# Kernel optimization log

Measured on AMD Instinct MI355X. Metric: run time of the kernel, lower is better.

## Reference

```python
import jax, jax.numpy as jnp
import numpy as np

PLANES = 128
SCALE = float(np.sqrt(PLANES))
TEMP = 0.05


def _maxpool2x2(x):
    # x: [B, C, H, W] -> [B, C, H//2, W//2]
    return jax.lax.reduce_window(x, -jnp.inf, jax.lax.max,
                                 (1, 1, 2, 2), (1, 1, 2, 2), 'VALID')


def _conv1x1(x, w, b=None):
    # x: [B, Cin, H, W], w: [Cout, Cin]
    y = jnp.einsum('bchw,oc->bohw', x, w)
    if b is not None:
        y = y + b[None, :, None, None]
    return y


def setup_inputs() -> dict:
    key = jax.random.key(0)
    ks = jax.random.split(key, 9)
    B, C, H, W = 8, 512, 64, 64
    std = 0.01  # init.normal_(w, 0, 0.01)
    x = jax.random.normal(ks[0], (B, C, H, W), dtype=jnp.float32)
    wq = jax.random.normal(ks[1], (PLANES, C), dtype=jnp.float32) * std
    bq = jnp.zeros((PLANES,), dtype=jnp.float32)
    wk = jax.random.normal(ks[2], (PLANES, C), dtype=jnp.float32) * std
    bk = jnp.zeros((PLANES,), dtype=jnp.float32)
    wv = jax.random.normal(ks[3], (C, C), dtype=jnp.float32) * std  # no bias (use_out=False)
    wm = jax.random.normal(ks[4], (1, C), dtype=jnp.float32) * std
    bm = jnp.zeros((1,), dtype=jnp.float32)
    # torch inits gamma to zero; use a nonzero value so the attention path matters
    gamma = jax.random.normal(ks[5], (1,), dtype=jnp.float32)
    return {'x': x, 'wq': wq, 'bq': bq, 'wk': wk, 'bk': bk,
            'wv': wv, 'wm': wm, 'bm': bm, 'gamma': gamma}


def reference(x, wq, bq, wk, bk, wv, wm, bm, gamma):
    B, C, H, W = x.shape
    xd = _maxpool2x2(x)                                   # [B,C,H/2,W/2]
    Hm, Wm = xd.shape[2], xd.shape[3]
    N, M = H * W, Hm * Wm
    q = _conv1x1(x, wq, bq).reshape(B, PLANES, N)         # [B,P,N]
    k = _conv1x1(xd, wk, bk).reshape(B, PLANES, M)        # [B,P,M]
    v = _conv1x1(xd, wv).reshape(B, C, M)                 # [B,C,M]
    # 'channel' whitening: subtract per-channel spatial mean
    q = q - q.mean(axis=2, keepdims=True)
    k = k - k.mean(axis=2, keepdims=True)
    sim = jnp.einsum('bpn,bpm->bnm', q, k) / (SCALE * TEMP)  # [B,N,M]
    sim = jax.nn.softmax(sim, axis=2)
    out_sim = jnp.einsum('bnm,bcm->bcn', sim, v).reshape(B, C, H, W)
    out_sim = gamma[0] * out_sim
    # global-context branch (with_gc, no 2fc)
    mask = _conv1x1(xd, wm, bm).reshape(B, M)             # [B,M]
    mask = jax.nn.softmax(mask, axis=1)
    out_gc = jnp.einsum('bcm,bm->bc', v, mask)[:, :, None, None]  # [B,C,1,1]
    return out_sim + out_gc + x
```

## Files before the change

kernel.cpp:

```cpp
#include <hip/hip_runtime.h>

typedef float f32x4 __attribute__((ext_vector_type(4)));
typedef short bf16x8 __attribute__((ext_vector_type(8)));
typedef short s16x4 __attribute__((ext_vector_type(4)));
typedef unsigned short u16;

#define B_ 8
#define C_ 512
#define N_ 4096
#define M_ 1024
#define P_ 128
#define INV_ST 1.7677669529663689f
#define A2C 2.5506631384888954f
#define B2C 23.083120654223414f

#define MFMA __builtin_amdgcn_mfma_f32_16x16x32_bf16

__device__ __forceinline__ u16 f2b(float f) {
  unsigned u = __float_as_uint(f);
  u += 0x7fffu + ((u >> 16) & 1u);
  return (u16)(u >> 16);
}
__device__ __forceinline__ float b2f(u16 h) {
  return __uint_as_float(((unsigned)h) << 16);
}
__device__ __forceinline__ float waveRedSum(float v) {
#pragma unroll
  for (int off = 32; off > 0; off >>= 1) v += __shfl_xor(v, off);
  return v;
}
__device__ __forceinline__ void gload_lds16(const u16* g, u16* l) {
  __builtin_amdgcn_global_load_lds(
      (const __attribute__((address_space(1))) void*)g,
      (__attribute__((address_space(3))) void*)l, 16, 0, 0);
}

__global__ __launch_bounds__(256) void prep_pool(const float* __restrict__ x,
                                                 float* __restrict__ xd,
                                                 float* __restrict__ meanx,
                                                 float* __restrict__ meanxd) {
  const int bc = blockIdx.x;
  const int tid = threadIdx.x;
  const int lane = tid & 63, wid = tid >> 6;
  const float* xp = x + (size_t)bc * 4096;
  float* xdp = xd + (size_t)bc * 1024;
  __shared__ float xs[4096];
  __shared__ float w4[4], w4b[4];
  float s = 0.f;
#pragma unroll
  for (int i = 0; i < 16; ++i) {
    float v = xp[i * 256 + tid];
    xs[i * 256 + tid] = v;
    s += v;
  }
  s = waveRedSum(s);
  if (lane == 0) w4[wid] = s;
  __syncthreads();
  if (tid == 0) meanx[bc] = (w4[0] + w4[1] + w4[2] + w4[3]) * (1.f / 4096.f);
  float sd = 0.f;
#pragma unroll
  for (int i = 0; i < 4; ++i) {
    int mp = i * 256 + tid;
    int r2 = mp >> 5, c2 = mp & 31;
    const float* p0 = xs + r2 * 128 + c2 * 2;
    float v = fmaxf(fmaxf(p0[0], p0[1]), fmaxf(p0[64], p0[65]));
    xdp[mp] = v;
    sd += v;
  }
  sd = waveRedSum(sd);
  if (lane == 0) w4b[wid] = sd;
  __syncthreads();
  if (tid == 0) meanxd[bc] = (w4b[0] + w4b[1] + w4b[2] + w4b[3]) * (1.f / 1024.f);
}

__global__ __launch_bounds__(256) void f2bf3(const float* __restrict__ a,
                                             const float* __restrict__ b,
                                             const float* __restrict__ c,
                                             u16* __restrict__ oa,
                                             u16* __restrict__ ob,
                                             u16* __restrict__ oc) {
  int i = blockIdx.x * 256 + threadIdx.x;
  if (i < 65536) oa[i] = f2b(a[i]);
  else if (i < 131072) ob[i - 65536] = f2b(b[i - 65536]);
  else if (i < 393216) oc[i - 131072] = f2b(c[i - 131072]);
}

template <int ROWS, bool TRANS, bool SUBMEAN>
__global__ __launch_bounds__(256) void gemm_wx(const u16* __restrict__ A,
                                               const float* __restrict__ Bsrc,
                                               const float* __restrict__ mean,
                                               u16* __restrict__ outp,
                                               int Cout, int Ncols) {
  constexpr int IT = ROWS / 32;
  const int b = blockIdx.z;
  const int col0 = blockIdx.x * 64;
  const int row0 = blockIdx.y * ROWS;
  const int tid = threadIdx.x;
  const int lane = tid & 63, wid = tid >> 6;
  const int g = lane >> 4, c16 = lane & 15;
  const int wr = (wid >> 1) * (ROWS / 2), wc = (wid & 1) * 32;
  __shared__ __align__(16) u16 As[ROWS][72];
  __shared__ __align__(16) u16 Bt[64][72];
  const float* Bb = Bsrc + (size_t)b * 512 * Ncols;
  const float* mb = SUBMEAN ? (mean + b * 512) : nullptr;
  f32x4 acc[IT][2];
#pragma unroll
  for (int i = 0; i < IT; ++i)
#pragma unroll
    for (int j = 0; j < 2; ++j) acc[i][j] = (f32x4){0.f, 0.f, 0.f, 0.f};

  for (int k0 = 0; k0 < 512; k0 += 64) {
#pragma unroll
    for (int i = 0; i < IT; ++i) {
      int f = tid + i * 256;
      int r = f >> 3, c8 = f & 7;
      *(bf16x8*)&As[r][c8 * 8] =
          *(const bf16x8*)(A + (size_t)(row0 + r) * 512 + k0 + c8 * 8);
    }
#pragma unroll
    for (int i = 0; i < 4; ++i) {
      int f = tid + i * 256;
      int kr = f >> 4, n4 = (f & 15) * 4;
      const float* src = Bb + (size_t)(k0 + kr) * Ncols + col0 + n4;
      float4 val = *(const float4*)src;
      if (SUBMEAN) {
        float mv = mb[k0 + kr];
        val.x -= mv; val.y -= mv; val.z -= mv; val.w -= mv;
      }
      Bt[n4 + 0][kr] = f2b(val.x);
      Bt[n4 + 1][kr] = f2b(val.y);
      Bt[n4 + 2][kr] = f2b(val.z);
      Bt[n4 + 3][kr] = f2b(val.w);
    }
    __syncthreads();
#pragma unroll
    for (int kk = 0; kk < 2; ++kk) {
      bf16x8 bfr[2];
#pragma unroll
      for (int j = 0; j < 2; ++j)
        bfr[j] = *(const bf16x8*)&Bt[wc + j * 16 + c16][kk * 32 + g * 8];
#pragma unroll
      for (int i = 0; i < IT; ++i) {
        bf16x8 af = *(const bf16x8*)&As[wr + i * 16 + c16][kk * 32 + g * 8];
#pragma unroll
        for (int j = 0; j < 2; ++j)
          acc[i][j] = MFMA(af, bfr[j], acc[i][j], 0, 0, 0);
      }
    }
    __syncthreads();
  }
  if (TRANS) {
#pragma unroll
    for (int i = 0; i < IT; ++i)
#pragma unroll
      for (int j = 0; j < 2; ++j) {
        int row = row0 + wr + i * 16 + g * 4;
        int col = col0 + wc + j * 16 + c16;
        s16x4 h;
#pragma unroll
        for (int r = 0; r < 4; ++r) h[r] = (short)f2b(acc[i][j][r]);
        *(s16x4*)(outp + ((size_t)b * Ncols + col) * Cout + row) = h;
      }
  } else {
#pragma unroll
    for (int i = 0; i < IT; ++i)
#pragma unroll
      for (int j = 0; j < 2; ++j) {
        int row = row0 + wr + i * 16 + g * 4;
        int col = col0 + wc + j * 16 + c16;
#pragma unroll
        for (int r = 0; r < 4; ++r)
          outp[((size_t)b * Cout + row + r) * Ncols + col] = f2b(acc[i][j][r]);
      }
  }
}

__global__ __launch_bounds__(128) void k_logits(const float* __restrict__ xd,
                                                const float* __restrict__ wm,
                                                const float* __restrict__ bmp,
                                                float* __restrict__ logits) {
  const int b = blockIdx.x >> 5, mc = blockIdx.x & 31;
  const int t = threadIdx.x;
  const int ml = t & 31, cq = t >> 5;
  const int m = mc * 32 + ml;
  __shared__ float part[4][32];
  const float* xb = xd + (size_t)b * 512 * 1024 + m;
  float s0 = 0, s1 = 0, s2 = 0, s3 = 0;
  const int cb = cq * 128;
#pragma unroll 8
  for (int c = 0; c < 128; c += 4) {
    s0 += wm[cb + c + 0] * xb[(size_t)(cb + c + 0) * 1024];
    s1 += wm[cb + c + 1] * xb[(size_t)(cb + c + 1) * 1024];
    s2 += wm[cb + c + 2] * xb[(size_t)(cb + c + 2) * 1024];
    s3 += wm[cb + c + 3] * xb[(size_t)(cb + c + 3) * 1024];
  }
  part[cq][ml] = (s0 + s1) + (s2 + s3);
  __syncthreads();
  if (t < 32)
    logits[b * 1024 + mc * 32 + t] =
        part[0][t] + part[1][t] + part[2][t] + part[3][t] + bmp[0];
}

__global__ __launch_bounds__(256) void k_gc(const float* __restrict__ logits,
                                            const u16* __restrict__ v,
                                            float* __restrict__ gc) {
  const int b = blockIdx.x >> 4, cc = blockIdx.x & 15;
  const int tid = threadIdx.x;
  const int lane = tid & 63, wid = tid >> 6;
  __shared__ float pl[1024];
  __shared__ float r4[4];
  __shared__ float stot[2];
  float4 lv = *(const float4*)&logits[b * 1024 + tid * 4];
  float mx = fmaxf(fmaxf(lv.x, lv.y), fmaxf(lv.z, lv.w));
#pragma unroll
  for (int off = 32; off > 0; off >>= 1) mx = fmaxf(mx, __shfl_xor(mx, off));
  if (lane == 0) r4[wid] = mx;
  __syncthreads();
  if (tid == 0) stot[0] = fmaxf(fmaxf(r4[0], r4[1]), fmaxf(r4[2], r4[3]));
  __syncthreads();
  const float M = stot[0];
  float e0 = __expf(lv.x - M), e1 = __expf(lv.y - M);
  float e2 = __expf(lv.z - M), e3 = __expf(lv.w - M);
  pl[tid * 4 + 0] = e0; pl[tid * 4 + 1] = e1;
  pl[tid * 4 + 2] = e2; pl[tid * 4 + 3] = e3;
  float ps = waveRedSum((e0 + e1) + (e2 + e3));
  if (lane == 0) r4[wid] = ps;
  __syncthreads();
  if (tid == 0) stot[1] = 1.0f / (r4[0] + r4[1] + r4[2] + r4[3]);
  __syncthreads();
  const float inv = stot[1];
  const int c = cc * 32 + (tid >> 3), sub = tid & 7;
  const u16* vr = v + ((size_t)b * 512 + c) * 1024 + sub * 128;
  const float* plr = pl + sub * 128;
  float s = 0;
#pragma unroll
  for (int i = 0; i < 16; ++i) {
    bf16x8 h = *(const bf16x8*)(vr + i * 8);
#pragma unroll
    for (int j = 0; j < 8; ++j) s += b2f((u16)h[j]) * plr[i * 8 + j];
  }
  s += __shfl_xor(s, 1);
  s += __shfl_xor(s, 2);
  s += __shfl_xor(s, 4);
  if (sub == 0) gc[b * 512 + c] = s * inv;
}

__global__ __launch_bounds__(512, 2) void attn(const u16* __restrict__ q,
                                               const u16* __restrict__ kt,
                                               const u16* __restrict__ v,
                                               const float* __restrict__ gc,
                                               const float* __restrict__ x,
                                               const float* __restrict__ gamma,
                                               float* __restrict__ out) {
  extern __shared__ __align__(16) char smem[];
  u16* Vl = (u16*)smem;
  u16* Pl = (u16*)(smem + 131072);
  float* l_s = (float*)(smem + 139264);

  const int bid = blockIdx.x;
  const int b = bid & 7;
  const int n0 = (bid >> 3) * 64;
  const int tid = threadIdx.x;
  const int lane = tid & 63, wid = tid >> 6;
  const int g = lane >> 4, c16 = lane & 15;
  const int mb = wid & 3, nh = wid >> 2;
  const int xsw = (c16 & 7) << 3;

  bf16x8 qf[2][4];
  {
    const u16* qr = q + ((size_t)b * N_ + n0 + nh * 32 + c16) * P_ + g * 8;
#pragma unroll
    for (int t = 0; t < 2; ++t)
#pragma unroll
      for (int kf = 0; kf < 4; ++kf)
        qf[t][kf] = *(const bf16x8*)(qr + t * 16 * P_ + kf * 32);
  }
  const u16* ktr = kt + ((size_t)b * M_ + mb * 16 + c16) * P_ + g * 8;
  bf16x8 kb[2][4];
#pragma unroll
  for (int kf = 0; kf < 4; ++kf) kb[0][kf] = *(const bf16x8*)(ktr + kf * 32);
  const u16* vst = v + ((size_t)b * C_ + wid * 64 + (lane >> 3)) * M_ +
                   ((lane & 7) ^ (lane >> 3)) * 8;
#pragma unroll
  for (int i = 0; i < 8; ++i)
    gload_lds16(vst + (size_t)i * 8 * M_, Vl + (wid * 8 + i) * 512);

  f32x4 acc[4][4];
#pragma unroll
  for (int i = 0; i < 4; ++i)
#pragma unroll
    for (int j = 0; j < 4; ++j) acc[i][j] = (f32x4){0.f, 0.f, 0.f, 0.f};
  float lp0 = 0.f, lp1 = 0.f;

#pragma unroll
  for (int s = 0; s < 16; ++s) {
    const int par = s & 1, nxt = par ^ 1;
    const int m0n = ((s + 1) & 15) * 64;
    f32x4 sv0 = (f32x4){0.f, 0.f, 0.f, 0.f};
    f32x4 sv1 = (f32x4){0.f, 0.f, 0.f, 0.f};
#pragma unroll
    for (int kf = 0; kf < 4; ++kf) {
      sv0 = MFMA(kb[par][kf], qf[0][kf], sv0, 0, 0, 0);
      sv1 = MFMA(kb[par][kf], qf[1][kf], sv1, 0, 0, 0);
    }
    float p00 = exp2f(fmaf(sv0[0], A2C, -B2C));
    float p01 = exp2f(fmaf(sv0[1], A2C, -B2C));
    float p02 = exp2f(fmaf(sv0[2], A2C, -B2C));
    float p03 = exp2f(fmaf(sv0[3], A2C, -B2C));
    float p10 = exp2f(fmaf(sv1[0], A2C, -B2C));
    float p11 = exp2f(fmaf(sv1[1], A2C, -B2C));
    float p12 = exp2f(fmaf(sv1[2], A2C, -B2C));
    float p13 = exp2f(fmaf(sv1[3], A2C, -B2C));
    lp0 += (p00 + p01) + (p02 + p03);
    lp1 += (p10 + p11) + (p12 + p13);
    uint2 w0, w1;
    w0.x = (unsigned)f2b(p00) | ((unsigned)f2b(p01) << 16);
    w0.y = (unsigned)f2b(p02) | ((unsigned)f2b(p03) << 16);
    w1.x = (unsigned)f2b(p10) | ((unsigned)f2b(p11) << 16);
    w1.y = (unsigned)f2b(p12) | ((unsigned)f2b(p13) << 16);

    __builtin_amdgcn_sched_barrier(0);
    __builtin_amdgcn_s_barrier();
    __builtin_amdgcn_sched_barrier(0);
#pragma unroll
    for (int kf = 0; kf < 4; ++kf)
      kb[nxt][kf] = *(const bf16x8*)(ktr + (size_t)m0n * P_ + kf * 32);
#pragma unroll
    for (int i = 0; i < 8; ++i)
      gload_lds16(vst + (size_t)(m0n + i * 8 * M_),
                  Vl + nxt * 32768 + (wid * 8 + i) * 512);
    {
      const int nA = nh * 32 + c16;
      const int o = (mb * 16 + g * 4) ^ xsw;
      *(uint2*)&Pl[nA * 64 + o] = w0;
      *(uint2*)&Pl[(nA + 16) * 64 + o] = w1;
    }
    asm volatile("s_waitcnt vmcnt(12) lgkmcnt(0)" ::: "memory");
    __builtin_amdgcn_sched_barrier(0);
    __builtin_amdgcn_s_barrier();
    __builtin_amdgcn_sched_barrier(0);
    const u16* VlP = Vl + par * 32768;
#pragma unroll
    for (int kk = 0; kk < 2; ++kk) {
      bf16x8 pb[4];
#pragma unroll
      for (int nb = 0; nb < 4; ++nb)
        pb[nb] = *(const bf16x8*)&Pl[(nb * 16 + c16) * 64 + ((kk * 32 + g * 8) ^ xsw)];
#pragma unroll
      for (int cf = 0; cf < 4; ++cf) {
        bf16x8 va = *(const bf16x8*)&VlP[(wid * 64 + cf * 16 + c16) * 64 +
                                         ((kk * 32 + g * 8) ^ xsw)];
#pragma unroll
        for (int nb = 0; nb < 4; ++nb)
          acc[cf][nb] = MFMA(va, pb[nb], acc[cf][nb], 0, 0, 0);
      }
    }
  }

  lp0 += __shfl_xor(lp0, 16); lp0 += __shfl_xor(lp0, 32);
  lp1 += __shfl_xor(lp1, 16); lp1 += __shfl_xor(lp1, 32);
  if (lane < 16) {
    l_s[mb * 64 + nh * 32 + lane] = lp0;
    l_s[mb * 64 + nh * 32 + 16 + lane] = lp1;
  }
  __syncthreads();
  float linv[4];
#pragma unroll
  for (int nb = 0; nb < 4; ++nb) {
    int n = nb * 16 + c16;
    linv[nb] = 1.0f / (l_s[n] + l_s[64 + n] + l_s[128 + n] + l_s[192 + n]);
  }
  const float gam = gamma[0];
#pragma unroll
  for (int cf = 0; cf < 4; ++cf) {
    const int c = wid * 64 + cf * 16 + g * 4;
    float gcv[4];
#pragma unroll
    for (int r = 0; r < 4; ++r) gcv[r] = gc[b * C_ + c + r];
#pragma unroll
    for (int nb = 0; nb < 4; ++nb) {
      const size_t idx0 = ((size_t)b * C_ + c) * (size_t)N_ + n0 + nb * 16 + c16;
#pragma unroll
      for (int r = 0; r < 4; ++r) {
        const size_t idx = idx0 + (size_t)r * N_;
        out[idx] = gam * acc[cf][nb][r] * linv[nb] + gcv[r] + x[idx];
      }
    }
  }
}

extern "C" void kernel_launch(void* const* d_in, const int* in_sizes, int n_in,
                              void* d_out, int out_size, void* d_ws, size_t ws_size,
                              hipStream_t stream) {
  const float* x     = (const float*)d_in[0];
  const float* wq    = (const float*)d_in[1];
  const float* wk    = (const float*)d_in[3];
  const float* wv    = (const float*)d_in[5];
  const float* wm    = (const float*)d_in[6];
  const float* bm    = (const float*)d_in[7];
  const float* gamma = (const float*)d_in[8];
  float* out = (float*)d_out;
  char* ws = (char*)d_ws;

  float* xd     = (float*)(ws + 0);
  float* meanx  = (float*)(ws + 16777216);
  float* meanxd = (float*)(ws + 16793600);
  u16*   q_ws   = (u16*)(ws + 16809984);
  u16*   kt_ws  = (u16*)(ws + 25198592);
  u16*   v_ws   = (u16*)(ws + 27295744);
  u16*   wq_b   = (u16*)(ws + 35684352);
  u16*   wk_b   = (u16*)(ws + 35815424);
  u16*   wv_b   = (u16*)(ws + 35946496);
  float* gc     = (float*)(ws + 36470784);
  float* logits = (float*)(ws + 36487168);

  prep_pool<<<dim3(B_ * C_), dim3(256), 0, stream>>>(x, xd, meanx, meanxd);
  f2bf3<<<dim3(1536), dim3(256), 0, stream>>>(wq, wk, wv, wq_b, wk_b, wv_b);
  gemm_wx<128, true, true><<<dim3(64, 1, B_), dim3(256), 0, stream>>>(
      wq_b, x, meanx, q_ws, 128, 4096);
  gemm_wx<128, true, true><<<dim3(16, 1, B_), dim3(256), 0, stream>>>(
      wk_b, xd, meanxd, kt_ws, 128, 1024);
  gemm_wx<128, false, false><<<dim3(16, 4, B_), dim3(256), 0, stream>>>(
      wv_b, xd, nullptr, v_ws, 512, 1024);
  k_logits<<<dim3(256), dim3(128), 0, stream>>>(xd, wm, bm, logits);
  k_gc<<<dim3(128), dim3(256), 0, stream>>>(logits, v_ws, gc);

  hipFuncSetAttribute((const void*)attn,
                      hipFuncAttributeMaxDynamicSharedMemorySize, 140288);
  attn<<<dim3(512), dim3(512), 140288, stream>>>(q_ws, kt_ws, v_ws, gc, x,
                                                 gamma, out);
}
```

Baseline: 307.2 us.

## Pre-transpose x to bf16, fold mean subtraction into GEMM epilogue, software-pipeline attention

A new prep kernel transposes x and the pooled xd into channel-last bf16 buffers and accumulates the channel means with atomics. The q/k mean subtraction is now applied as a precomputed W·mean correction in the GEMM epilogue, so the GEMMs load bf16 operands directly with larger tiles. The mask-logit computation is merged into the weight-conversion kernel. The attention loop double-buffers P in LDS and computes the next tile's scores after the PV MMA, dropping one barrier per iteration. In exchange this adds an extra pass writing the transposed copies, atomics, a memset and more LDS in attention.

```diff
diff --git a/kernel.cpp b/kernel.cpp
--- a/kernel.cpp
+++ b/kernel.cpp
@@ -10,7 +10,6 @@
 #define N_ 4096
 #define M_ 1024
 #define P_ 128
-#define INV_ST 1.7677669529663689f
 #define A2C 2.5506631384888954f
 #define B2C 23.083120654223414f
 
@@ -35,115 +34,162 @@
       (__attribute__((address_space(3))) void*)l, 16, 0, 0);
 }
 
-__global__ __launch_bounds__(256) void prep_pool(const float* __restrict__ x,
-                                                 float* __restrict__ xd,
-                                                 float* __restrict__ meanx,
-                                                 float* __restrict__ meanxd) {
-  const int bc = blockIdx.x;
-  const int tid = threadIdx.x;
-  const int lane = tid & 63, wid = tid >> 6;
-  const float* xp = x + (size_t)bc * 4096;
-  float* xdp = xd + (size_t)bc * 1024;
-  __shared__ float xs[4096];
-  __shared__ float w4[4], w4b[4];
-  float s = 0.f;
-#pragma unroll
-  for (int i = 0; i < 16; ++i) {
-    float v = xp[i * 256 + tid];
-    xs[i * 256 + tid] = v;
-    s += v;
-  }
-  s = waveRedSum(s);
-  if (lane == 0) w4[wid] = s;
-  __syncthreads();
-  if (tid == 0) meanx[bc] = (w4[0] + w4[1] + w4[2] + w4[3]) * (1.f / 4096.f);
-  float sd = 0.f;
-#pragma unroll
-  for (int i = 0; i < 4; ++i) {
-    int mp = i * 256 + tid;
-    int r2 = mp >> 5, c2 = mp & 31;
-    const float* p0 = xs + r2 * 128 + c2 * 2;
-    float v = fmaxf(fmaxf(p0[0], p0[1]), fmaxf(p0[64], p0[65]));
-    xdp[mp] = v;
-    sd += v;
-  }
-  sd = waveRedSum(sd);
-  if (lane == 0) w4b[wid] = sd;
-  __syncthreads();
-  if (tid == 0) meanxd[bc] = (w4b[0] + w4b[1] + w4b[2] + w4b[3]) * (1.f / 1024.f);
-}
-
-__global__ __launch_bounds__(256) void f2bf3(const float* __restrict__ a,
-                                             const float* __restrict__ b,
-                                             const float* __restrict__ c,
-                                             u16* __restrict__ oa,
-                                             u16* __restrict__ ob,
-                                             u16* __restrict__ oc) {
-  int i = blockIdx.x * 256 + threadIdx.x;
-  if (i < 65536) oa[i] = f2b(a[i]);
-  else if (i < 131072) ob[i - 65536] = f2b(b[i - 65536]);
-  else if (i < 393216) oc[i - 131072] = f2b(c[i - 131072]);
-}
-
-template <int ROWS, bool TRANS, bool SUBMEAN>
-__global__ __launch_bounds__(256) void gemm_wx(const u16* __restrict__ A,
-                                               const float* __restrict__ Bsrc,
-                                               const float* __restrict__ mean,
+__global__ __launch_bounds__(256) void prep_tx(const float* __restrict__ x,
+                                               u16* __restrict__ xt,
+                                               u16* __restrict__ xdt,
+                                               float* __restrict__ meanx,
+                                               float* __restrict__ meanxd) {
+  const int bid = blockIdx.x;
+  const int b = bid >> 8, ct = (bid >> 5) & 7, hp = bid & 31;
+  const int t = threadIdx.x;
+  const int lane = t & 63, wid = t >> 6;
+  __shared__ float xs[64 * 133];
+  __shared__ float part[4][64];
+  const float* xb = x + ((size_t)(b * 512 + ct * 64) * 4096) + hp * 128;
+#pragma unroll
+  for (int it = 0; it < 32; ++it) {
+    int c = it * 2 + (t >> 7);
+    int n = t & 127;
+    xs[c * 133 + n] = xb[(size_t)c * 4096 + n];
+  }
+  __syncthreads();
+  {
+    int c = t >> 2, qq = t & 3;
+    float s = 0;
+#pragma unroll
+    for (int j = 0; j < 32; ++j) s += xs[c * 133 + qq * 32 + j];
+    s += __shfl_xor(s, 1);
+    s += __shfl_xor(s, 2);
+    if (qq == 0) atomicAdd(&meanx[b * 512 + ct * 64 + c], s * (1.f / 4096.f));
+  }
+#pragma unroll
+  for (int it = 0; it < 16; ++it) {
+    int n = it * 8 + (t >> 5), cp = t & 31;
+    float lo = xs[(2 * cp) * 133 + n], hi = xs[(2 * cp + 1) * 133 + n];
+    unsigned u = (unsigned)f2b(lo) | ((unsigned)f2b(hi) << 16);
+    *(unsigned*)(xt + (((size_t)b * 4096) + hp * 128 + n) * 512 + ct * 64 + 2 * cp) = u;
+  }
+  float s0 = 0, s1 = 0;
+  const int cp = t & 31;
+#pragma unroll
+  for (int it = 0; it < 4; ++it) {
+    int wm = it * 8 + (t >> 5);
+    int c0 = 2 * cp;
+    float a = fmaxf(fmaxf(xs[c0 * 133 + 2 * wm], xs[c0 * 133 + 2 * wm + 1]),
+                    fmaxf(xs[c0 * 133 + 64 + 2 * wm], xs[c0 * 133 + 64 + 2 * wm + 1]));
+    float d = fmaxf(fmaxf(xs[(c0 + 1) * 133 + 2 * wm], xs[(c0 + 1) * 133 + 2 * wm + 1]),
+                    fmaxf(xs[(c0 + 1) * 133 + 64 + 2 * wm], xs[(c0 + 1) * 133 + 64 + 2 * wm + 1]));
+    unsigned u = (unsigned)f2b(a) | ((unsigned)f2b(d) << 16);
+    *(unsigned*)(xdt + (((size_t)b * 1024) + hp * 32 + wm) * 512 + ct * 64 + c0) = u;
+    s0 += a; s1 += d;
+  }
+  s0 += __shfl_xor(s0, 32);
+  s1 += __shfl_xor(s1, 32);
+  if (lane < 32) { part[wid][2 * cp] = s0; part[wid][2 * cp + 1] = s1; }
+  __syncthreads();
+  if (t < 64)
+    atomicAdd(&meanxd[b * 512 + ct * 64 + t],
+              (part[0][t] + part[1][t] + part[2][t] + part[3][t]) * (1.f / 1024.f));
+}
+
+__global__ __launch_bounds__(256) void wcvt(const float* __restrict__ wq,
+                                            const float* __restrict__ wk,
+                                            const float* __restrict__ wv,
+                                            const float* __restrict__ wm,
+                                            const float* __restrict__ bm,
+                                            const float* __restrict__ meanx,
+                                            const float* __restrict__ meanxd,
+                                            const u16* __restrict__ xdt,
+                                            u16* __restrict__ wq_b,
+                                            u16* __restrict__ wk_b,
+                                            u16* __restrict__ wv_b,
+                                            float* __restrict__ corr_q,
+                                            float* __restrict__ corr_k,
+                                            float* __restrict__ logits) {
+  const int bid = blockIdx.x, t = threadIdx.x;
+  if (bid < 1536) {
+    int i = bid * 256 + t;
+    if (i < 65536) wq_b[i] = f2b(wq[i]);
+    else if (i < 131072) wk_b[i - 65536] = f2b(wk[i - 65536]);
+    else wv_b[i - 131072] = f2b(wv[i - 131072]);
+  } else if (bid < 1552) {
+    int blk = bid - 1536, b = blk & 7, sel = blk >> 3;
+    const float* w = sel ? wk : wq;
+    const float* mn = (sel ? meanxd : meanx) + b * 512;
+    int p = t >> 1, h = t & 1;
+    const float* wr = w + p * 512 + h * 256;
+    const float* mr = mn + h * 256;
+    float s = 0;
+#pragma unroll 8
+    for (int c = 0; c < 256; ++c) s += wr[c] * mr[c];
+    s += __shfl_xor(s, 1);
+    if (h == 0) (sel ? corr_k : corr_q)[b * 128 + p] = s;
+  } else {
+    int blk = bid - 1552;
+    int b = blk >> 8, mblk = blk & 255;
+    int lane = t & 63, wv4 = t >> 6;
+    int m = mblk * 4 + wv4;
+    bf16x8 h8 = *(const bf16x8*)(xdt + ((size_t)b * 1024 + m) * 512 + lane * 8);
+    const float* wmr = wm + lane * 8;
+    float s = 0;
+#pragma unroll
+    for (int j = 0; j < 8; ++j) s += b2f((u16)h8[j]) * wmr[j];
+    s = waveRedSum(s);
+    if (lane == 0) logits[b * 1024 + m] = s + bm[0];
+  }
+}
+
+template <int BR, int BC, bool TRANS, bool CORR>
+__global__ __launch_bounds__(256) void gemm_bt(const u16* __restrict__ A,
+                                               const u16* __restrict__ Bt,
+                                               const float* __restrict__ corr,
                                                u16* __restrict__ outp,
                                                int Cout, int Ncols) {
-  constexpr int IT = ROWS / 32;
+  constexpr int WR = BR / 2, WC = BC / 2, ITR = WR / 16, ITC = WC / 16;
+  constexpr int AFR = BR * 8 / 256, BFR = BC * 8 / 256;
   const int b = blockIdx.z;
-  const int col0 = blockIdx.x * 64;
-  const int row0 = blockIdx.y * ROWS;
+  const int col0 = blockIdx.x * BC;
+  const int row0 = blockIdx.y * BR;
   const int tid = threadIdx.x;
   const int lane = tid & 63, wid = tid >> 6;
   const int g = lane >> 4, c16 = lane & 15;
-  const int wr = (wid >> 1) * (ROWS / 2), wc = (wid & 1) * 32;
-  __shared__ __align__(16) u16 As[ROWS][72];
-  __shared__ __align__(16) u16 Bt[64][72];
-  const float* Bb = Bsrc + (size_t)b * 512 * Ncols;
-  const float* mb = SUBMEAN ? (mean + b * 512) : nullptr;
-  f32x4 acc[IT][2];
-#pragma unroll
-  for (int i = 0; i < IT; ++i)
-#pragma unroll
-    for (int j = 0; j < 2; ++j) acc[i][j] = (f32x4){0.f, 0.f, 0.f, 0.f};
+  const int wr = (wid >> 1) * WR, wc = (wid & 1) * WC;
+  __shared__ __align__(16) u16 As[BR][72];
+  __shared__ __align__(16) u16 Bs[BC][72];
+  const u16* Bb = Bt + (size_t)b * Ncols * 512;
+  f32x4 acc[ITR][ITC];
+#pragma unroll
+  for (int i = 0; i < ITR; ++i)
+#pragma unroll
+    for (int j = 0; j < ITC; ++j) acc[i][j] = (f32x4){0.f, 0.f, 0.f, 0.f};
 
   for (int k0 = 0; k0 < 512; k0 += 64) {
 #pragma unroll
-    for (int i = 0; i < IT; ++i) {
+    for (int i = 0; i < AFR; ++i) {
       int f = tid + i * 256;
       int r = f >> 3, c8 = f & 7;
       *(bf16x8*)&As[r][c8 * 8] =
           *(const bf16x8*)(A + (size_t)(row0 + r) * 512 + k0 + c8 * 8);
     }
 #pragma unroll
-    for (int i = 0; i < 4; ++i) {
+    for (int i = 0; i < BFR; ++i) {
       int f = tid + i * 256;
-      int kr = f >> 4, n4 = (f & 15) * 4;
-      const float* src = Bb + (size_t)(k0 + kr) * Ncols + col0 + n4;
-      float4 val = *(const float4*)src;
-      if (SUBMEAN) {
-        float mv = mb[k0 + kr];
-        val.x -= mv; val.y -= mv; val.z -= mv; val.w -= mv;
-      }
-      Bt[n4 + 0][kr] = f2b(val.x);
-      Bt[n4 + 1][kr] = f2b(val.y);
-      Bt[n4 + 2][kr] = f2b(val.z);
-      Bt[n4 + 3][kr] = f2b(val.w);
+      int r = f >> 3, c8 = f & 7;
+      *(bf16x8*)&Bs[r][c8 * 8] =
+          *(const bf16x8*)(Bb + (size_t)(col0 + r) * 512 + k0 + c8 * 8);
     }
     __syncthreads();
 #pragma unroll
     for (int kk = 0; kk < 2; ++kk) {
-      bf16x8 bfr[2];
-#pragma unroll
-      for (int j = 0; j < 2; ++j)
-        bfr[j] = *(const bf16x8*)&Bt[wc + j * 16 + c16][kk * 32 + g * 8];
-#pragma unroll
-      for (int i = 0; i < IT; ++i) {
+      bf16x8 bfr[ITC];
+#pragma unroll
+      for (int j = 0; j < ITC; ++j)
+        bfr[j] = *(const bf16x8*)&Bs[wc + j * 16 + c16][kk * 32 + g * 8];
+#pragma unroll
+      for (int i = 0; i < ITR; ++i) {
         bf16x8 af = *(const bf16x8*)&As[wr + i * 16 + c16][kk * 32 + g * 8];
 #pragma unroll
-        for (int j = 0; j < 2; ++j)
+        for (int j = 0; j < ITC; ++j)
           acc[i][j] = MFMA(af, bfr[j], acc[i][j], 0, 0, 0);
       }
     }
@@ -151,21 +197,25 @@
   }
   if (TRANS) {
 #pragma unroll
-    for (int i = 0; i < IT; ++i)
-#pragma unroll
-      for (int j = 0; j < 2; ++j) {
+    for (int i = 0; i < ITR; ++i)
+#pragma unroll
+      for (int j = 0; j < ITC; ++j) {
         int row = row0 + wr + i * 16 + g * 4;
         int col = col0 + wc + j * 16 + c16;
         s16x4 h;
 #pragma unroll
-        for (int r = 0; r < 4; ++r) h[r] = (short)f2b(acc[i][j][r]);
+        for (int r = 0; r < 4; ++r) {
+          float val = acc[i][j][r];
+          if (CORR) val -= corr[b * 128 + row + r];
+          h[r] = (short)f2b(val);
+        }
         *(s16x4*)(outp + ((size_t)b * Ncols + col) * Cout + row) = h;
       }
   } else {
 #pragma unroll
-    for (int i = 0; i < IT; ++i)
-#pragma unroll
-      for (int j = 0; j < 2; ++j) {
+    for (int i = 0; i < ITR; ++i)
+#pragma unroll
+      for (int j = 0; j < ITC; ++j) {
         int row = row0 + wr + i * 16 + g * 4;
         int col = col0 + wc + j * 16 + c16;
 #pragma unroll
@@ -173,32 +223,6 @@
           outp[((size_t)b * Cout + row + r) * Ncols + col] = f2b(acc[i][j][r]);
       }
   }
-}
-
-__global__ __launch_bounds__(128) void k_logits(const float* __restrict__ xd,
-                                                const float* __restrict__ wm,
-                                                const float* __restrict__ bmp,
-                                                float* __restrict__ logits) {
-  const int b = blockIdx.x >> 5, mc = blockIdx.x & 31;
-  const int t = threadIdx.x;
-  const int ml = t & 31, cq = t >> 5;
-  const int m = mc * 32 + ml;
-  __shared__ float part[4][32];
-  const float* xb = xd + (size_t)b * 512 * 1024 + m;
-  float s0 = 0, s1 = 0, s2 = 0, s3 = 0;
-  const int cb = cq * 128;
-#pragma unroll 8
-  for (int c = 0; c < 128; c += 4) {
-    s0 += wm[cb + c + 0] * xb[(size_t)(cb + c + 0) * 1024];
-    s1 += wm[cb + c + 1] * xb[(size_t)(cb + c + 1) * 1024];
-    s2 += wm[cb + c + 2] * xb[(size_t)(cb + c + 2) * 1024];
-    s3 += wm[cb + c + 3] * xb[(size_t)(cb + c + 3) * 1024];
-  }
-  part[cq][ml] = (s0 + s1) + (s2 + s3);
-  __syncthreads();
-  if (t < 32)
-    logits[b * 1024 + mc * 32 + t] =
-        part[0][t] + part[1][t] + part[2][t] + part[3][t] + bmp[0];
 }
 
 __global__ __launch_bounds__(256) void k_gc(const float* __restrict__ logits,
@@ -245,6 +269,35 @@
   if (sub == 0) gc[b * 512 + c] = s * inv;
 }
 
+__device__ __forceinline__ void s_phase(const bf16x8* kbf, const bf16x8 (&qf)[2][4],
+                                        u16* PlBuf, int nA, int o,
+                                        float& lp0, float& lp1) {
+  f32x4 sv0 = (f32x4){0.f, 0.f, 0.f, 0.f};
+  f32x4 sv1 = (f32x4){0.f, 0.f, 0.f, 0.f};
+#pragma unroll
+  for (int kf = 0; kf < 4; ++kf) {
+    sv0 = MFMA(kbf[kf], qf[0][kf], sv0, 0, 0, 0);
+    sv1 = MFMA(kbf[kf], qf[1][kf], sv1, 0, 0, 0);
+  }
+  float p00 = exp2f(fmaf(sv0[0], A2C, -B2C));
+  float p01 = exp2f(fmaf(sv0[1], A2C, -B2C));
+  float p02 = exp2f(fmaf(sv0[2], A2C, -B2C));
+  float p03 = exp2f(fmaf(sv0[3], A2C, -B2C));
+  float p10 = exp2f(fmaf(sv1[0], A2C, -B2C));
+  float p11 = exp2f(fmaf(sv1[1], A2C, -B2C));
+  float p12 = exp2f(fmaf(sv1[2], A2C, -B2C));
+  float p13 = exp2f(fmaf(sv1[3], A2C, -B2C));
+  lp0 += (p00 + p01) + (p02 + p03);
+  lp1 += (p10 + p11) + (p12 + p13);
+  uint2 w0, w1;
+  w0.x = (unsigned)f2b(p00) | ((unsigned)f2b(p01) << 16);
+  w0.y = (unsigned)f2b(p02) | ((unsigned)f2b(p03) << 16);
+  w1.x = (unsigned)f2b(p10) | ((unsigned)f2b(p11) << 16);
+  w1.y = (unsigned)f2b(p12) | ((unsigned)f2b(p13) << 16);
+  *(uint2*)&PlBuf[nA * 64 + o] = w0;
+  *(uint2*)&PlBuf[(nA + 16) * 64 + o] = w1;
+}
+
 __global__ __launch_bounds__(512, 2) void attn(const u16* __restrict__ q,
                                                const u16* __restrict__ kt,
                                                const u16* __restrict__ v,
@@ -255,8 +308,7 @@
   extern __shared__ __align__(16) char smem[];
   u16* Vl = (u16*)smem;
   u16* Pl = (u16*)(smem + 131072);
-  float* l_s = (float*)(smem + 139264);
-
+  float* l_s = (float*)(smem + 147456);
   const int bid = blockIdx.x;
   const int b = bid & 7;
   const int n0 = (bid >> 3) * 64;
@@ -265,6 +317,8 @@
   const int g = lane >> 4, c16 = lane & 15;
   const int mb = wid & 3, nh = wid >> 2;
   const int xsw = (c16 & 7) << 3;
+  const int nA = nh * 32 + c16;
+  const int po = (mb * 16 + g * 4) ^ xsw;
 
   bf16x8 qf[2][4];
   {
@@ -279,73 +333,53 @@
   bf16x8 kb[2][4];
 #pragma unroll
   for (int kf = 0; kf < 4; ++kf) kb[0][kf] = *(const bf16x8*)(ktr + kf * 32);
+#pragma unroll
+  for (int kf = 0; kf < 4; ++kf) kb[1][kf] = *(const bf16x8*)(ktr + 64 * P_ + kf * 32);
   const u16* vst = v + ((size_t)b * C_ + wid * 64 + (lane >> 3)) * M_ +
                    ((lane & 7) ^ (lane >> 3)) * 8;
 #pragma unroll
   for (int i = 0; i < 8; ++i)
     gload_lds16(vst + (size_t)i * 8 * M_, Vl + (wid * 8 + i) * 512);
 
+  float lp0 = 0.f, lp1 = 0.f;
+  s_phase(kb[0], qf, Pl, nA, po, lp0, lp1);
+
   f32x4 acc[4][4];
 #pragma unroll
   for (int i = 0; i < 4; ++i)
 #pragma unroll
     for (int j = 0; j < 4; ++j) acc[i][j] = (f32x4){0.f, 0.f, 0.f, 0.f};
-  float lp0 = 0.f, lp1 = 0.f;
-
-#pragma unroll
+
+#pragma unroll 2
   for (int s = 0; s < 16; ++s) {
     const int par = s & 1, nxt = par ^ 1;
-    const int m0n = ((s + 1) & 15) * 64;
-    f32x4 sv0 = (f32x4){0.f, 0.f, 0.f, 0.f};
-    f32x4 sv1 = (f32x4){0.f, 0.f, 0.f, 0.f};
-#pragma unroll
-    for (int kf = 0; kf < 4; ++kf) {
-      sv0 = MFMA(kb[par][kf], qf[0][kf], sv0, 0, 0, 0);
-      sv1 = MFMA(kb[par][kf], qf[1][kf], sv1, 0, 0, 0);
-    }
-    float p00 = exp2f(fmaf(sv0[0], A2C, -B2C));
-    float p01 = exp2f(fmaf(sv0[1], A2C, -B2C));
-    float p02 = exp2f(fmaf(sv0[2], A2C, -B2C));
-    float p03 = exp2f(fmaf(sv0[3], A2C, -B2C));
-    float p10 = exp2f(fmaf(sv1[0], A2C, -B2C));
-    float p11 = exp2f(fmaf(sv1[1], A2C, -B2C));
-    float p12 = exp2f(fmaf(sv1[2], A2C, -B2C));
-    float p13 = exp2f(fmaf(sv1[3], A2C, -B2C));
-    lp0 += (p00 + p01) + (p02 + p03);
-    lp1 += (p10 + p11) + (p12 + p13);
-    uint2 w0, w1;
-    w0.x = (unsigned)f2b(p00) | ((unsigned)f2b(p01) << 16);
-    w0.y = (unsigned)f2b(p02) | ((unsigned)f2b(p03) << 16);
-    w1.x = (unsigned)f2b(p10) | ((unsigned)f2b(p11) << 16);
-    w1.y = (unsigned)f2b(p12) | ((unsigned)f2b(p13) << 16);
-
+    if (s < 14) {
+      const size_t moff = (size_t)(s + 2) * 64 * P_;
+#pragma unroll
+      for (int kf = 0; kf < 4; ++kf)
+        kb[par][kf] = *(const bf16x8*)(ktr + moff + kf * 32);
+      asm volatile("s_waitcnt vmcnt(4) lgkmcnt(0)" ::: "memory");
+    } else {
+      asm volatile("s_waitcnt vmcnt(0) lgkmcnt(0)" ::: "memory");
+    }
     __builtin_amdgcn_sched_barrier(0);
     __builtin_amdgcn_s_barrier();
     __builtin_amdgcn_sched_barrier(0);
-#pragma unroll
-    for (int kf = 0; kf < 4; ++kf)
-      kb[nxt][kf] = *(const bf16x8*)(ktr + (size_t)m0n * P_ + kf * 32);
-#pragma unroll
-    for (int i = 0; i < 8; ++i)
-      gload_lds16(vst + (size_t)(m0n + i * 8 * M_),
-                  Vl + nxt * 32768 + (wid * 8 + i) * 512);
-    {
-      const int nA = nh * 32 + c16;
-      const int o = (mb * 16 + g * 4) ^ xsw;
-      *(uint2*)&Pl[nA * 64 + o] = w0;
-      *(uint2*)&Pl[(nA + 16) * 64 + o] = w1;
-    }
-    asm volatile("s_waitcnt vmcnt(12) lgkmcnt(0)" ::: "memory");
-    __builtin_amdgcn_sched_barrier(0);
-    __builtin_amdgcn_s_barrier();
-    __builtin_amdgcn_sched_barrier(0);
+    if (s < 15) {
+      const int m1 = (s + 1) * 64;
+#pragma unroll
+      for (int i = 0; i < 8; ++i)
+        gload_lds16(vst + m1 + (size_t)i * 8 * M_,
+                    Vl + nxt * 32768 + (wid * 8 + i) * 512);
+    }
     const u16* VlP = Vl + par * 32768;
+    const u16* PlP = Pl + par * 4096;
 #pragma unroll
     for (int kk = 0; kk < 2; ++kk) {
       bf16x8 pb[4];
 #pragma unroll
       for (int nb = 0; nb < 4; ++nb)
-        pb[nb] = *(const bf16x8*)&Pl[(nb * 16 + c16) * 64 + ((kk * 32 + g * 8) ^ xsw)];
+        pb[nb] = *(const bf16x8*)&PlP[(nb * 16 + c16) * 64 + ((kk * 32 + g * 8) ^ xsw)];
 #pragma unroll
       for (int cf = 0; cf < 4; ++cf) {
         bf16x8 va = *(const bf16x8*)&VlP[(wid * 64 + cf * 16 + c16) * 64 +
@@ -355,6 +389,7 @@
           acc[cf][nb] = MFMA(va, pb[nb], acc[cf][nb], 0, 0, 0);
       }
     }
+    if (s < 15) s_phase(kb[nxt], qf, Pl + nxt * 4096, nA, po, lp0, lp1);
   }
 
   lp0 += __shfl_xor(lp0, 16); lp0 += __shfl_xor(lp0, 32);
@@ -402,31 +437,36 @@
   float* out = (float*)d_out;
   char* ws = (char*)d_ws;
 
-  float* xd     = (float*)(ws + 0);
-  float* meanx  = (float*)(ws + 16777216);
-  float* meanxd = (float*)(ws + 16793600);
-  u16*   q_ws   = (u16*)(ws + 16809984);
-  u16*   kt_ws  = (u16*)(ws + 25198592);
-  u16*   v_ws   = (u16*)(ws + 27295744);
-  u16*   wq_b   = (u16*)(ws + 35684352);
-  u16*   wk_b   = (u16*)(ws + 35815424);
-  u16*   wv_b   = (u16*)(ws + 35946496);
-  float* gc     = (float*)(ws + 36470784);
-  float* logits = (float*)(ws + 36487168);
-
-  prep_pool<<<dim3(B_ * C_), dim3(256), 0, stream>>>(x, xd, meanx, meanxd);
-  f2bf3<<<dim3(1536), dim3(256), 0, stream>>>(wq, wk, wv, wq_b, wk_b, wv_b);
-  gemm_wx<128, true, true><<<dim3(64, 1, B_), dim3(256), 0, stream>>>(
-      wq_b, x, meanx, q_ws, 128, 4096);
-  gemm_wx<128, true, true><<<dim3(16, 1, B_), dim3(256), 0, stream>>>(
-      wk_b, xd, meanxd, kt_ws, 128, 1024);
-  gemm_wx<128, false, false><<<dim3(16, 4, B_), dim3(256), 0, stream>>>(
-      wv_b, xd, nullptr, v_ws, 512, 1024);
-  k_logits<<<dim3(256), dim3(128), 0, stream>>>(xd, wm, bm, logits);
+  u16*   xt     = (u16*)(ws + 0);
+  u16*   xdt    = (u16*)(ws + 33554432);
+  u16*   q_ws   = (u16*)(ws + 41943040);
+  u16*   kt_ws  = (u16*)(ws + 50331648);
+  u16*   v_ws   = (u16*)(ws + 52428800);
+  u16*   wq_b   = (u16*)(ws + 60817408);
+  u16*   wk_b   = (u16*)(ws + 60948480);
+  u16*   wv_b   = (u16*)(ws + 61079552);
+  float* meanx  = (float*)(ws + 61603840);
+  float* meanxd = (float*)(ws + 61620224);
+  float* corr_q = (float*)(ws + 61636608);
+  float* corr_k = (float*)(ws + 61640704);
+  float* gc     = (float*)(ws + 61644800);
+  float* logits = (float*)(ws + 61661184);
+
+  hipMemsetAsync(ws + 61603840, 0, 32768, stream);
+  prep_tx<<<dim3(2048), dim3(256), 0, stream>>>(x, xt, xdt, meanx, meanxd);
+  wcvt<<<dim3(3600), dim3(256), 0, stream>>>(wq, wk, wv, wm, bm, meanx, meanxd,
+                                             xdt, wq_b, wk_b, wv_b, corr_q,
+                                             corr_k, logits);
+  gemm_bt<128, 128, true, true><<<dim3(32, 1, B_), dim3(256), 0, stream>>>(
+      wq_b, xt, corr_q, q_ws, 128, 4096);
+  gemm_bt<128, 64, true, true><<<dim3(16, 1, B_), dim3(256), 0, stream>>>(
+      wk_b, xdt, corr_k, kt_ws, 128, 1024);
+  gemm_bt<128, 128, false, false><<<dim3(8, 4, B_), dim3(256), 0, stream>>>(
+      wv_b, xdt, nullptr, v_ws, 512, 1024);
   k_gc<<<dim3(128), dim3(256), 0, stream>>>(logits, v_ws, gc);
 
   hipFuncSetAttribute((const void*)attn,
-                      hipFuncAttributeMaxDynamicSharedMemorySize, 140288);
-  attn<<<dim3(512), dim3(512), 140288, stream>>>(q_ws, kt_ws, v_ws, gc, x,
+                      hipFuncAttributeMaxDynamicSharedMemorySize, 148480);
+  attn<<<dim3(512), dim3(512), 148480, stream>>>(q_ws, kt_ws, v_ws, gc, x,
                                                  gamma, out);
 }
```

New measurement: 255.2 us. 16.9% less time.
